# Kernel tuning notes

Hardware: AMD Instinct MI355X
Metric: run time of the kernel (lower is better)

The kernel has to match this reference:

```python
import jax, jax.numpy as jnp
import numpy as np

BLOCK = 128
QMAX = 127.0


def _quant_dequant_act(x2d):
    """Dynamic per-token, per-128-column-group INT8 quantize + dequantize.

    x2d: [T, K]. Groups of shape 1x128 along K (is_weight=False path).
    """
    T, K = x2d.shape
    xb = x2d.reshape(T, K // BLOCK, BLOCK)
    amax = jnp.max(jnp.abs(xb), axis=-1, keepdims=True)
    scale = jnp.where(amax > 0, amax / QMAX, 1.0)
    q = jnp.clip(jnp.round(xb / scale), -QMAX, QMAX)  # int8 values
    return (q * scale).reshape(T, K)


def _quant_dequant_weight(w):
    """128x128 blockwise INT8 quantize + dequantize (is_weight=True path).

    w: [O, K] with O, K multiples of 128.
    """
    O, K = w.shape
    wb = w.reshape(O // BLOCK, BLOCK, K // BLOCK, BLOCK)
    amax = jnp.max(jnp.abs(wb), axis=(1, 3), keepdims=True)
    scale = jnp.where(amax > 0, amax / QMAX, 1.0)
    q = jnp.clip(jnp.round(wb / scale), -QMAX, QMAX)
    return (q * scale).reshape(O, K)


def setup_inputs() -> dict:
    key = jax.random.key(0)
    k1, k2, k3 = jax.random.split(key, 3)
    B, S, K, O = 4, 2048, 4096, 11008
    x = jax.random.normal(k1, (B, S, K), dtype=jnp.float32)
    w = jax.random.normal(k2, (O, K), dtype=jnp.float32) * 0.02
    bias = jax.random.normal(k3, (O,), dtype=jnp.float32) * 0.01
    return {"x": x, "w": w, "bias": bias}


def reference(x, w, bias):
    """INT8Linear forward: dynamic per-token INT8 activation quantization +
    128x128 blockwise-scaled INT8 weight GEMM + bias.

    Because scales are constant within each (token-group x weight-block),
    the blockwise-scaled int8 GEMM is mathematically identical to
    dequantize-then-matmul, which is the efficient dense expression here.
    """
    in_shape = x.shape
    x2d = x.reshape(-1, in_shape[-1])        # [T, K]
    xdq = _quant_dequant_act(x2d)            # [T, K]
    wdq = _quant_dequant_weight(w)           # [O, K]
    y = jnp.einsum('tk,ok->to', xdq, wdq) + bias
    return y.reshape(*in_shape[:-1], w.shape[0])
```

## Files before the change

kernel.cpp:

```cpp
#include <hip/hip_runtime.h>
#include <hip/hip_bf16.h>
#include <stdint.h>

#define QMAXF 127.0f

typedef __attribute__((ext_vector_type(8))) short bf16x8;
typedef __attribute__((ext_vector_type(4))) float f32x4;

typedef __attribute__((address_space(1))) void gbl_void;
typedef __attribute__((address_space(3))) void lds_void;

__device__ __forceinline__ void gload_lds16(const void* g, void* l) {
    __builtin_amdgcn_global_load_lds((const gbl_void*)g, (lds_void*)l, 16, 0, 0);
}

__device__ __forceinline__ unsigned short f2bf(float f) {
    unsigned int u = __builtin_bit_cast(unsigned int, f);
    unsigned int r = (u + 0x7fffu + ((u >> 16) & 1u)) >> 16;
    return (unsigned short)r;
}

__global__ __launch_bounds__(256) void qd_x_kernel(const float* __restrict__ x,
                                                   unsigned short* __restrict__ xdq,
                                                   long ngroups) {
    long gw = ((long)blockIdx.x * blockDim.x + threadIdx.x) >> 6;
    int lane = threadIdx.x & 63;
    if (gw >= ngroups) return;

    float2 v = *(reinterpret_cast<const float2*>(x) + gw * 64 + lane);
    float a = fmaxf(fabsf(v.x), fabsf(v.y));
#pragma unroll
    for (int off = 32; off; off >>= 1) a = fmaxf(a, __shfl_xor(a, off));

    float scale = a > 0.f ? a / QMAXF : 1.f;
    float qx = fminf(fmaxf(rintf(v.x / scale), -QMAXF), QMAXF);
    float qy = fminf(fmaxf(rintf(v.y / scale), -QMAXF), QMAXF);
    unsigned int packed = (unsigned int)f2bf(qx * scale) | ((unsigned int)f2bf(qy * scale) << 16);
    reinterpret_cast<unsigned int*>(xdq)[gw * 64 + lane] = packed;
}

__global__ __launch_bounds__(256) void qd_w_kernel(const float* __restrict__ w,
                                                   unsigned short* __restrict__ wdq,
                                                   int K) {
    int kb = blockIdx.x, ob = blockIdx.y;
    size_t base = (size_t)ob * 128 * K + (size_t)kb * 128;
    int t = threadIdx.x;

    float4 v[16];
    float a = 0.f;
#pragma unroll
    for (int i = 0; i < 16; i++) {
        int f = i * 256 + t;
        int row = f >> 5, c4 = f & 31;
        v[i] = *reinterpret_cast<const float4*>(w + base + (size_t)row * K + c4 * 4);
        a = fmaxf(a, fmaxf(fmaxf(fabsf(v[i].x), fabsf(v[i].y)),
                           fmaxf(fabsf(v[i].z), fabsf(v[i].w))));
    }
#pragma unroll
    for (int off = 32; off; off >>= 1) a = fmaxf(a, __shfl_xor(a, off));

    __shared__ float red[4];
    if ((t & 63) == 0) red[t >> 6] = a;
    __syncthreads();
    a = fmaxf(fmaxf(red[0], red[1]), fmaxf(red[2], red[3]));

    float scale = a > 0.f ? a / QMAXF : 1.f;
#pragma unroll
    for (int i = 0; i < 16; i++) {
        int f = i * 256 + t;
        int row = f >> 5, c4 = f & 31;
        float q0 = fminf(fmaxf(rintf(v[i].x / scale), -QMAXF), QMAXF);
        float q1 = fminf(fmaxf(rintf(v[i].y / scale), -QMAXF), QMAXF);
        float q2 = fminf(fmaxf(rintf(v[i].z / scale), -QMAXF), QMAXF);
        float q3 = fminf(fmaxf(rintf(v[i].w / scale), -QMAXF), QMAXF);
        uint2 p;
        p.x = (unsigned int)f2bf(q0 * scale) | ((unsigned int)f2bf(q1 * scale) << 16);
        p.y = (unsigned int)f2bf(q2 * scale) | ((unsigned int)f2bf(q3 * scale) << 16);
        *reinterpret_cast<uint2*>(wdq + base + (size_t)row * K + c4 * 4) = p;
    }
}

#define GBM 256
#define GBN 256
#define GBK 64
#define TILE_SH (GBM * GBK)
#define SLOT_SH (2 * TILE_SH)

#define BAR()                              \
    do {                                   \
        asm volatile("" ::: "memory");     \
        __builtin_amdgcn_s_barrier();      \
        asm volatile("" ::: "memory");     \
    } while (0)
#define WAITL0()                                          \
    do {                                                  \
        asm volatile("s_waitcnt lgkmcnt(0)" ::: "memory");\
        __builtin_amdgcn_sched_barrier(0);                \
    } while (0)
#define WAITV(n) asm volatile("s_waitcnt vmcnt(" #n ")" ::: "memory")
#define SCHED0() __builtin_amdgcn_sched_barrier(0)

__global__ __launch_bounds__(512, 1) void gemm8p_kernel(
    const unsigned short* __restrict__ A,
    const unsigned short* __restrict__ Bw,
    const float* __restrict__ bias,
    float* __restrict__ C,
    int M, int N, int K) {
    __shared__ alignas(16) unsigned short lds[2 * SLOT_SH];

    int nTm = M / GBM, nTn = N / GBN;
    int nwg = gridDim.x, wg = blockIdx.x;
    int mt, nt;
    if ((nTm & 7) == 0 && (32 % (nTm >> 3)) == 0) {
        int x = wg & 7, j = wg >> 3;
        int mper = nTm >> 3;
        int G = 32 / mper;
        int wsz = mper * G;
        int fullw = nTn / G;
        int jfull = fullw * wsz;
        int g, r, width;
        if (j < jfull) { g = j / wsz; r = j - g * wsz; width = G; }
        else { g = fullw; r = j - jfull; width = nTn - fullw * G; }
        mt = x * mper + r / width;
        nt = g * G + r % width;
    } else {
        int swz = (nwg & 7) ? wg : ((wg & 7) * (nwg >> 3) + (wg >> 3));
        mt = swz / nTn; nt = swz - mt * nTn;
    }

    int t = threadIdx.x, wid = t >> 6, lane = t & 63;
    int wm = wid >> 2, wn = wid & 3;
    int lr = lane & 15, lq = lane >> 4;

    const unsigned short* Abase = A + (size_t)mt * GBM * K;
    const unsigned short* Bbase = Bw + (size_t)nt * GBN * K;

    int r0 = t >> 3;
    int pc = t & 7;
    int c0 = pc ^ (r0 & 7);
    const unsigned short* Aln = Abase + (size_t)r0 * K + c0 * 8;
    const unsigned short* Bln = Bbase + (size_t)r0 * K + c0 * 8;

    auto STAGE = [&](int slot, int mat, int half, int kb) {
        const unsigned short* g = (mat ? Bln : Aln) + (size_t)half * 128 * K + kb;
        unsigned short* d = &lds[slot * SLOT_SH + mat * TILE_SH + (half * 1024 + t) * 8];
        gload_lds16(g, d);
        gload_lds16(g + (size_t)64 * K, d + 512 * 8);
    };

    int xo0 = lq ^ (lr & 7);
    int xo1 = (4 + lq) ^ (lr & 7);
    int offA[4][2], offB[2][2];
#pragma unroll
    for (int m = 0; m < 4; m++) {
        int row = wm * 128 + m * 16 + lr;
        offA[m][0] = (row * 8 + xo0) * 8;
        offA[m][1] = (row * 8 + xo1) * 8;
    }
#pragma unroll
    for (int n = 0; n < 2; n++) {
        int row = wn * 64 + n * 16 + lr;
        offB[n][0] = TILE_SH + (row * 8 + xo0) * 8;
        offB[n][1] = TILE_SH + (row * 8 + xo1) * 8;
    }

    f32x4 acc[8][4];
#pragma unroll
    for (int m = 0; m < 8; m++)
#pragma unroll
        for (int n = 0; n < 4; n++) acc[m][n] = (f32x4){0.f, 0.f, 0.f, 0.f};

    bf16x8 arE[8], arO[8], b0[4], b1[4];

    auto LD_A = [&](int slot, int mq, bf16x8* ar) {
        int base = slot * SLOT_SH + mq * 4096;
#pragma unroll
        for (int m = 0; m < 4; m++)
#pragma unroll
            for (int kk = 0; kk < 2; kk++)
                ar[m * 2 + kk] = *reinterpret_cast<const bf16x8*>(&lds[base + offA[m][kk]]);
    };
    auto LD_B = [&](int slot, int nq, bf16x8* b) {
        int base = slot * SLOT_SH + nq * 2048;
#pragma unroll
        for (int n = 0; n < 2; n++)
#pragma unroll
            for (int kk = 0; kk < 2; kk++)
                b[n * 2 + kk] = *reinterpret_cast<const bf16x8*>(&lds[base + offB[n][kk]]);
    };
    auto MMA = [&](int mq, int nq, bf16x8* ar, bf16x8* b) {
        __builtin_amdgcn_s_setprio(1);
#pragma unroll
        for (int m = 0; m < 4; m++)
#pragma unroll
            for (int n = 0; n < 2; n++)
#pragma unroll
                for (int kk = 0; kk < 2; kk++)
                    acc[mq * 4 + m][nq * 2 + n] = __builtin_amdgcn_mfma_f32_16x16x32_bf16(
                        ar[m * 2 + kk], b[n * 2 + kk], acc[mq * 4 + m][nq * 2 + n], 0, 0, 0);
        __builtin_amdgcn_s_setprio(0);
    };

    int NTm1 = K / GBK - 1;
    int NI = (K / GBK) / 2;

    STAGE(0, 0, 0, 0);
    STAGE(0, 0, 1, 0);
    STAGE(0, 1, 0, 0);
    STAGE(0, 1, 1, 0);
    STAGE(1, 1, 0, GBK);
    STAGE(1, 1, 1, GBK);
    WAITV(4);
    BAR();
    LD_A(0, 0, arE);
    LD_B(0, 0, b0);

    for (int i = 0; i < NI; ++i) {
        int kb1 = min(2 * i + 1, NTm1) * GBK;
        int kb2 = min(2 * i + 2, NTm1) * GBK;
        int kb3 = min(2 * i + 3, NTm1) * GBK;

        WAITL0();
        LD_B(0, 1, b1);
        STAGE(1, 0, 0, kb1);
        SCHED0();
        MMA(0, 0, arE, b0);
        BAR();
        WAITL0();
        LD_A(0, 1, arO);
        STAGE(1, 0, 1, kb1);
        SCHED0();
        MMA(0, 1, arE, b1);
        BAR();
        WAITL0();
        STAGE(0, 1, 0, kb2);
        SCHED0();
        MMA(1, 0, arO, b0);
        WAITV(2);
        BAR();
        WAITL0();
        LD_A(1, 0, arE);
        LD_B(1, 0, b0);
        STAGE(0, 1, 1, kb2);
        SCHED0();
        MMA(1, 1, arO, b1);
        BAR();
        WAITL0();
        LD_B(1, 1, b1);
        STAGE(0, 0, 0, kb2);
        SCHED0();
        MMA(0, 0, arE, b0);
        BAR();
        WAITL0();
        LD_A(1, 1, arO);
        STAGE(0, 0, 1, kb2);
        SCHED0();
        MMA(0, 1, arE, b1);
        BAR();
        WAITL0();
        STAGE(1, 1, 0, kb3);
        SCHED0();
        MMA(1, 0, arO, b0);
        WAITV(2);
        BAR();
        WAITL0();
        LD_A(0, 0, arE);
        LD_B(0, 0, b0);
        STAGE(1, 1, 1, kb3);
        SCHED0();
        MMA(1, 1, arO, b1);
        BAR();
    }

    float bvv[4];
#pragma unroll
    for (int n = 0; n < 4; n++) bvv[n] = bias[nt * GBN + wn * 64 + n * 16 + lr];

#pragma unroll
    for (int m = 0; m < 8; m++) {
#pragma unroll
        for (int r = 0; r < 4; r++) {
            size_t row = (size_t)(mt * GBM + wm * 128 + m * 16 + lq * 4 + r);
            float* Crow = C + row * N + nt * GBN + wn * 64 + lr;
#pragma unroll
            for (int n = 0; n < 4; n++) Crow[n * 16] = acc[m][n][r] + bvv[n];
        }
    }
}

extern "C" void kernel_launch(void* const* d_in, const int* in_sizes, int n_in,
                              void* d_out, int out_size, void* d_ws, size_t ws_size,
                              hipStream_t stream) {
    const float* x = (const float*)d_in[0];
    const float* w = (const float*)d_in[1];
    const float* bias = (const float*)d_in[2];
    float* y = (float*)d_out;

    int O = in_sizes[2];
    int K = in_sizes[1] / O;
    int T = in_sizes[0] / K;

    unsigned short* xdq = (unsigned short*)d_ws;
    size_t xbytes = ((size_t)T * K * 2 + 255) & ~(size_t)255;
    unsigned short* wdq = (unsigned short*)((char*)d_ws + xbytes);

    long ngroups = (long)T * (K / 128);
    qd_x_kernel<<<dim3((unsigned)((ngroups + 3) / 4)), dim3(256), 0, stream>>>(x, xdq, ngroups);
    qd_w_kernel<<<dim3(K / 128, O / 128), dim3(256), 0, stream>>>(w, wdq, K);

    int grid = (T / GBM) * (O / GBN);
    gemm8p_kernel<<<dim3(grid), dim3(512), 0, stream>>>(xdq, wdq, bias, y, T, O, K);
}
```

Baseline: 730.2 us.

## Replace bf16 dequantized GEMM with int8 MFMA GEMM and per-block scale fixup

The quantization kernels now store raw int8 values plus per-token-group and per-weight-block float scales, instead of dequantized bf16 tensors. The GEMM runs the K=128 quantization block as int32-accumulating i8 MFMAs. After each block it converts the partial sums to float and multiplies them by the activation and weight scales into float accumulators. This halves operand bytes and uses the higher int8 MFMA rate, in exchange for extra VALU conversion and FMA work per block. The pipeline is also simpler, with a full vmcnt drain each iteration, which may reduce load/compute overlap.

```diff
diff --git a/kernel.cpp b/kernel.cpp
--- a/kernel.cpp
+++ b/kernel.cpp
@@ -4,8 +4,8 @@
 
 #define QMAXF 127.0f
 
-typedef __attribute__((ext_vector_type(8))) short bf16x8;
 typedef __attribute__((ext_vector_type(4))) float f32x4;
+typedef __attribute__((ext_vector_type(4))) int i32x4;
 
 typedef __attribute__((address_space(1))) void gbl_void;
 typedef __attribute__((address_space(3))) void lds_void;
@@ -14,15 +14,10 @@
     __builtin_amdgcn_global_load_lds((const gbl_void*)g, (lds_void*)l, 16, 0, 0);
 }
 
-__device__ __forceinline__ unsigned short f2bf(float f) {
-    unsigned int u = __builtin_bit_cast(unsigned int, f);
-    unsigned int r = (u + 0x7fffu + ((u >> 16) & 1u)) >> 16;
-    return (unsigned short)r;
-}
-
 __global__ __launch_bounds__(256) void qd_x_kernel(const float* __restrict__ x,
-                                                   unsigned short* __restrict__ xdq,
-                                                   long ngroups) {
+                                                   char* __restrict__ qx,
+                                                   float* __restrict__ sxT,
+                                                   long ngroups, int nkb, int T) {
     long gw = ((long)blockIdx.x * blockDim.x + threadIdx.x) >> 6;
     int lane = threadIdx.x & 63;
     if (gw >= ngroups) return;
@@ -33,15 +28,21 @@
     for (int off = 32; off; off >>= 1) a = fmaxf(a, __shfl_xor(a, off));
 
     float scale = a > 0.f ? a / QMAXF : 1.f;
-    float qx = fminf(fmaxf(rintf(v.x / scale), -QMAXF), QMAXF);
-    float qy = fminf(fmaxf(rintf(v.y / scale), -QMAXF), QMAXF);
-    unsigned int packed = (unsigned int)f2bf(qx * scale) | ((unsigned int)f2bf(qy * scale) << 16);
-    reinterpret_cast<unsigned int*>(xdq)[gw * 64 + lane] = packed;
+    int q0 = (int)fminf(fmaxf(rintf(v.x / scale), -QMAXF), QMAXF);
+    int q1 = (int)fminf(fmaxf(rintf(v.y / scale), -QMAXF), QMAXF);
+    unsigned short packed = (unsigned short)((q0 & 0xFF) | ((q1 & 0xFF) << 8));
+    reinterpret_cast<unsigned short*>(qx)[gw * 64 + lane] = packed;
+
+    if (lane == 0) {
+        int t = (int)(gw / nkb), kb = (int)(gw - (long)t * nkb);
+        sxT[(size_t)kb * T + t] = scale;
+    }
 }
 
 __global__ __launch_bounds__(256) void qd_w_kernel(const float* __restrict__ w,
-                                                   unsigned short* __restrict__ wdq,
-                                                   int K) {
+                                                   char* __restrict__ qw,
+                                                   float* __restrict__ sw,
+                                                   int K, int nkb) {
     int kb = blockIdx.x, ob = blockIdx.y;
     size_t base = (size_t)ob * 128 * K + (size_t)kb * 128;
     int t = threadIdx.x;
@@ -65,26 +66,24 @@
     a = fmaxf(fmaxf(red[0], red[1]), fmaxf(red[2], red[3]));
 
     float scale = a > 0.f ? a / QMAXF : 1.f;
+    if (t == 0) sw[(size_t)ob * nkb + kb] = scale;
 #pragma unroll
     for (int i = 0; i < 16; i++) {
         int f = i * 256 + t;
         int row = f >> 5, c4 = f & 31;
-        float q0 = fminf(fmaxf(rintf(v[i].x / scale), -QMAXF), QMAXF);
-        float q1 = fminf(fmaxf(rintf(v[i].y / scale), -QMAXF), QMAXF);
-        float q2 = fminf(fmaxf(rintf(v[i].z / scale), -QMAXF), QMAXF);
-        float q3 = fminf(fmaxf(rintf(v[i].w / scale), -QMAXF), QMAXF);
-        uint2 p;
-        p.x = (unsigned int)f2bf(q0 * scale) | ((unsigned int)f2bf(q1 * scale) << 16);
-        p.y = (unsigned int)f2bf(q2 * scale) | ((unsigned int)f2bf(q3 * scale) << 16);
-        *reinterpret_cast<uint2*>(wdq + base + (size_t)row * K + c4 * 4) = p;
+        int q0 = (int)fminf(fmaxf(rintf(v[i].x / scale), -QMAXF), QMAXF);
+        int q1 = (int)fminf(fmaxf(rintf(v[i].y / scale), -QMAXF), QMAXF);
+        int q2 = (int)fminf(fmaxf(rintf(v[i].z / scale), -QMAXF), QMAXF);
+        int q3 = (int)fminf(fmaxf(rintf(v[i].w / scale), -QMAXF), QMAXF);
+        unsigned int p = (q0 & 0xFF) | ((q1 & 0xFF) << 8) | ((q2 & 0xFF) << 16) |
+                         ((unsigned int)(q3 & 0xFF) << 24);
+        *reinterpret_cast<unsigned int*>(qw + base + (size_t)row * K + c4 * 4) = p;
     }
 }
 
 #define GBM 256
 #define GBN 256
-#define GBK 64
-#define TILE_SH (GBM * GBK)
-#define SLOT_SH (2 * TILE_SH)
+#define SLOT_BY 65536
 
 #define BAR()                              \
     do {                                   \
@@ -97,16 +96,18 @@
         asm volatile("s_waitcnt lgkmcnt(0)" ::: "memory");\
         __builtin_amdgcn_sched_barrier(0);                \
     } while (0)
-#define WAITV(n) asm volatile("s_waitcnt vmcnt(" #n ")" ::: "memory")
+#define WAITV0() asm volatile("s_waitcnt vmcnt(0)" ::: "memory")
 #define SCHED0() __builtin_amdgcn_sched_barrier(0)
 
-__global__ __launch_bounds__(512, 1) void gemm8p_kernel(
-    const unsigned short* __restrict__ A,
-    const unsigned short* __restrict__ Bw,
+__global__ __launch_bounds__(512, 2) void gemm_i8_kernel(
+    const char* __restrict__ Aq,
+    const char* __restrict__ Bq,
+    const float* __restrict__ sxT,
+    const float* __restrict__ swp,
     const float* __restrict__ bias,
     float* __restrict__ C,
     int M, int N, int K) {
-    __shared__ alignas(16) unsigned short lds[2 * SLOT_SH];
+    __shared__ alignas(16) unsigned char lds8[2 * SLOT_BY];
 
     int nTm = M / GBM, nTn = N / GBN;
     int nwg = gridDim.x, wg = blockIdx.x;
@@ -131,144 +132,131 @@
     int t = threadIdx.x, wid = t >> 6, lane = t & 63;
     int wm = wid >> 2, wn = wid & 3;
     int lr = lane & 15, lq = lane >> 4;
-
-    const unsigned short* Abase = A + (size_t)mt * GBM * K;
-    const unsigned short* Bbase = Bw + (size_t)nt * GBN * K;
-
-    int r0 = t >> 3;
-    int pc = t & 7;
-    int c0 = pc ^ (r0 & 7);
-    const unsigned short* Aln = Abase + (size_t)r0 * K + c0 * 8;
-    const unsigned short* Bln = Bbase + (size_t)r0 * K + c0 * 8;
+    int nkb = K >> 7;
+
+    const char* Abase = Aq + (size_t)mt * GBM * K;
+    const char* Bbase = Bq + (size_t)nt * GBN * K;
+
+    int cid0 = t, cid1 = 512 + t;
+    int rl0 = cid0 >> 3, rl1 = cid1 >> 3;
+    int pc0 = cid0 & 7, pc1 = cid1 & 7;
+    int gc0 = (pc0 ^ (rl0 & 7)) * 16, gc1 = (pc1 ^ (rl1 & 7)) * 16;
 
     auto STAGE = [&](int slot, int mat, int half, int kb) {
-        const unsigned short* g = (mat ? Bln : Aln) + (size_t)half * 128 * K + kb;
-        unsigned short* d = &lds[slot * SLOT_SH + mat * TILE_SH + (half * 1024 + t) * 8];
-        gload_lds16(g, d);
-        gload_lds16(g + (size_t)64 * K, d + 512 * 8);
-    };
-
-    int xo0 = lq ^ (lr & 7);
-    int xo1 = (4 + lq) ^ (lr & 7);
+        const char* gb = (mat ? Bbase : Abase) + (size_t)(half * 128) * K + kb;
+        unsigned char* db = lds8 + slot * SLOT_BY + mat * 32768 + half * 16384;
+        gload_lds16(gb + (size_t)rl0 * K + gc0, db + cid0 * 16);
+        gload_lds16(gb + (size_t)rl1 * K + gc1, db + cid1 * 16);
+    };
+
     int offA[4][2], offB[2][2];
 #pragma unroll
     for (int m = 0; m < 4; m++) {
         int row = wm * 128 + m * 16 + lr;
-        offA[m][0] = (row * 8 + xo0) * 8;
-        offA[m][1] = (row * 8 + xo1) * 8;
+#pragma unroll
+        for (int kk = 0; kk < 2; kk++)
+            offA[m][kk] = row * 128 + (((kk * 4 + lq) ^ (lr & 7)) << 4);
     }
 #pragma unroll
     for (int n = 0; n < 2; n++) {
         int row = wn * 64 + n * 16 + lr;
-        offB[n][0] = TILE_SH + (row * 8 + xo0) * 8;
-        offB[n][1] = TILE_SH + (row * 8 + xo1) * 8;
-    }
-
-    f32x4 acc[8][4];
+#pragma unroll
+        for (int kk = 0; kk < 2; kk++)
+            offB[n][kk] = 32768 + row * 128 + (((kk * 4 + lq) ^ (lr & 7)) << 4);
+    }
+
+    f32x4 facc[8][4];
 #pragma unroll
     for (int m = 0; m < 8; m++)
 #pragma unroll
-        for (int n = 0; n < 4; n++) acc[m][n] = (f32x4){0.f, 0.f, 0.f, 0.f};
-
-    bf16x8 arE[8], arO[8], b0[4], b1[4];
-
-    auto LD_A = [&](int slot, int mq, bf16x8* ar) {
-        int base = slot * SLOT_SH + mq * 4096;
+        for (int n = 0; n < 4; n++) facc[m][n] = (f32x4){0.f, 0.f, 0.f, 0.f};
+
+    i32x4 a[4][2], b[2][2], ia[4][2];
+
+    auto LDA = [&](int slot, int mq) {
+        const unsigned char* base = lds8 + slot * SLOT_BY + mq * 8192;
 #pragma unroll
         for (int m = 0; m < 4; m++)
 #pragma unroll
             for (int kk = 0; kk < 2; kk++)
-                ar[m * 2 + kk] = *reinterpret_cast<const bf16x8*>(&lds[base + offA[m][kk]]);
-    };
-    auto LD_B = [&](int slot, int nq, bf16x8* b) {
-        int base = slot * SLOT_SH + nq * 2048;
+                a[m][kk] = *reinterpret_cast<const i32x4*>(base + offA[m][kk]);
+    };
+    auto LDB = [&](int slot, int nq) {
+        const unsigned char* base = lds8 + slot * SLOT_BY + nq * 4096;
 #pragma unroll
         for (int n = 0; n < 2; n++)
 #pragma unroll
             for (int kk = 0; kk < 2; kk++)
-                b[n * 2 + kk] = *reinterpret_cast<const bf16x8*>(&lds[base + offB[n][kk]]);
-    };
-    auto MMA = [&](int mq, int nq, bf16x8* ar, bf16x8* b) {
+                b[n][kk] = *reinterpret_cast<const i32x4*>(base + offB[n][kk]);
+    };
+    auto MMA = [&]() {
         __builtin_amdgcn_s_setprio(1);
 #pragma unroll
         for (int m = 0; m < 4; m++)
 #pragma unroll
-            for (int n = 0; n < 2; n++)
-#pragma unroll
-                for (int kk = 0; kk < 2; kk++)
-                    acc[mq * 4 + m][nq * 2 + n] = __builtin_amdgcn_mfma_f32_16x16x32_bf16(
-                        ar[m * 2 + kk], b[n * 2 + kk], acc[mq * 4 + m][nq * 2 + n], 0, 0, 0);
+            for (int n = 0; n < 2; n++) {
+                ia[m][n] = __builtin_amdgcn_mfma_i32_16x16x64_i8(
+                    a[m][0], b[n][0], (i32x4){0, 0, 0, 0}, 0, 0, 0);
+                ia[m][n] = __builtin_amdgcn_mfma_i32_16x16x64_i8(
+                    a[m][1], b[n][1], ia[m][n], 0, 0, 0);
+            }
         __builtin_amdgcn_s_setprio(0);
     };
-
-    int NTm1 = K / GBK - 1;
-    int NI = (K / GBK) / 2;
-
-    STAGE(0, 0, 0, 0);
-    STAGE(0, 0, 1, 0);
-    STAGE(0, 1, 0, 0);
-    STAGE(0, 1, 1, 0);
-    STAGE(1, 1, 0, GBK);
-    STAGE(1, 1, 1, GBK);
-    WAITV(4);
+    f32x4 sx4[4];
+    float sw;
+    auto FIX = [&](int mq, int nq) {
+#pragma unroll
+        for (int m = 0; m < 4; m++) {
+            f32x4 sxw = sx4[m] * sw;
+#pragma unroll
+            for (int n = 0; n < 2; n++) {
+                f32x4 cv;
+#pragma unroll
+                for (int r = 0; r < 4; r++) cv[r] = (float)ia[m][n][r];
+                facc[mq * 4 + m][nq * 2 + n] += cv * sxw;
+            }
+        }
+    };
+    int sxrow0 = mt * GBM + wm * 128 + lq * 4;
+    auto LDSX = [&](int i, int mq) {
+#pragma unroll
+        for (int m = 0; m < 4; m++)
+            sx4[m] = *reinterpret_cast<const f32x4*>(
+                sxT + (size_t)i * M + sxrow0 + mq * 64 + m * 16);
+    };
+
+    int swbase = (nt * 2 + (wn >> 1)) * nkb;
+
+    STAGE(0, 0, 0, 0); STAGE(0, 0, 1, 0);
+    STAGE(0, 1, 0, 0); STAGE(0, 1, 1, 0);
+    WAITV0();
     BAR();
-    LD_A(0, 0, arE);
-    LD_B(0, 0, b0);
-
-    for (int i = 0; i < NI; ++i) {
-        int kb1 = min(2 * i + 1, NTm1) * GBK;
-        int kb2 = min(2 * i + 2, NTm1) * GBK;
-        int kb3 = min(2 * i + 3, NTm1) * GBK;
-
-        WAITL0();
-        LD_B(0, 1, b1);
-        STAGE(1, 0, 0, kb1);
-        SCHED0();
-        MMA(0, 0, arE, b0);
+
+    for (int i = 0; i < nkb; ++i) {
+        int p = i & 1, q = p ^ 1;
+        int knext = (i + 1 < nkb ? i + 1 : i) * 128;
+
+        LDA(p, 0); LDB(p, 0);
+        STAGE(q, 0, 0, knext); STAGE(q, 1, 0, knext);
+        LDSX(i, 0);
+        sw = swp[swbase + i];
+        BAR(); WAITL0();
+        MMA(); FIX(0, 0);
         BAR();
-        WAITL0();
-        LD_A(0, 1, arO);
-        STAGE(1, 0, 1, kb1);
-        SCHED0();
-        MMA(0, 1, arE, b1);
+        LDB(p, 1);
+        STAGE(q, 0, 1, knext); STAGE(q, 1, 1, knext);
+        BAR(); WAITL0();
+        MMA(); FIX(0, 1);
         BAR();
-        WAITL0();
-        STAGE(0, 1, 0, kb2);
-        SCHED0();
-        MMA(1, 0, arO, b0);
-        WAITV(2);
+        LDA(p, 1);
+        LDSX(i, 1);
+        BAR(); WAITL0();
+        MMA(); FIX(1, 1);
         BAR();
-        WAITL0();
-        LD_A(1, 0, arE);
-        LD_B(1, 0, b0);
-        STAGE(0, 1, 1, kb2);
-        SCHED0();
-        MMA(1, 1, arO, b1);
-        BAR();
-        WAITL0();
-        LD_B(1, 1, b1);
-        STAGE(0, 0, 0, kb2);
-        SCHED0();
-        MMA(0, 0, arE, b0);
-        BAR();
-        WAITL0();
-        LD_A(1, 1, arO);
-        STAGE(0, 0, 1, kb2);
-        SCHED0();
-        MMA(0, 1, arE, b1);
-        BAR();
-        WAITL0();
-        STAGE(1, 1, 0, kb3);
-        SCHED0();
-        MMA(1, 0, arO, b0);
-        WAITV(2);
-        BAR();
-        WAITL0();
-        LD_A(0, 0, arE);
-        LD_B(0, 0, b0);
-        STAGE(1, 1, 1, kb3);
-        SCHED0();
-        MMA(1, 1, arO, b1);
+        LDB(p, 0);
+        BAR(); WAITL0();
+        MMA(); FIX(1, 0);
+        WAITV0();
         BAR();
     }
 
@@ -283,7 +271,7 @@
             size_t row = (size_t)(mt * GBM + wm * 128 + m * 16 + lq * 4 + r);
             float* Crow = C + row * N + nt * GBN + wn * 64 + lr;
 #pragma unroll
-            for (int n = 0; n < 4; n++) Crow[n * 16] = acc[m][n][r] + bvv[n];
+            for (int n = 0; n < 4; n++) Crow[n * 16] = facc[m][n][r] + bvv[n];
         }
     }
 }
@@ -299,15 +287,22 @@
     int O = in_sizes[2];
     int K = in_sizes[1] / O;
     int T = in_sizes[0] / K;
-
-    unsigned short* xdq = (unsigned short*)d_ws;
-    size_t xbytes = ((size_t)T * K * 2 + 255) & ~(size_t)255;
-    unsigned short* wdq = (unsigned short*)((char*)d_ws + xbytes);
-
-    long ngroups = (long)T * (K / 128);
-    qd_x_kernel<<<dim3((unsigned)((ngroups + 3) / 4)), dim3(256), 0, stream>>>(x, xdq, ngroups);
-    qd_w_kernel<<<dim3(K / 128, O / 128), dim3(256), 0, stream>>>(w, wdq, K);
+    int nkb = K / 128;
+
+    char* qx = (char*)d_ws;
+    size_t off = ((size_t)T * K + 255) & ~(size_t)255;
+    char* qw = (char*)d_ws + off;
+    off += ((size_t)O * K + 255) & ~(size_t)255;
+    float* sxT = (float*)((char*)d_ws + off);
+    off += ((size_t)nkb * T * 4 + 255) & ~(size_t)255;
+    float* sw = (float*)((char*)d_ws + off);
+
+    long ngroups = (long)T * nkb;
+    qd_x_kernel<<<dim3((unsigned)((ngroups + 3) / 4)), dim3(256), 0, stream>>>(
+        x, qx, sxT, ngroups, nkb, T);
+    qd_w_kernel<<<dim3(nkb, O / 128), dim3(256), 0, stream>>>(w, qw, sw, K, nkb);
 
     int grid = (T / GBM) * (O / GBN);
-    gemm8p_kernel<<<dim3(grid), dim3(512), 0, stream>>>(xdq, wdq, bias, y, T, O, K);
-}
+    gemm_i8_kernel<<<dim3(grid), dim3(512), 0, stream>>>(qx, qw, sxT, sw, bias, y,
+                                                         T, O, K);
+}
```

Measured after the change: 703.3 us. 3.7% less time.
